# Kernel tuning notes

Hardware: AMD Instinct MI355X
Metric: run time of the kernel (lower is better)

Reference implementation:

```python
import jax, jax.numpy as jnp
import numpy as np

DIM = 1024          # hidden_size
MOE_HID = 512       # moe_intermediate_size
SHARED_HID = 2048   # shared_expert_intermediate_size
N_EXPERTS = 16
TOP_K = 2
NORM_TOPK_PROB = True


def setup_inputs() -> dict:
    key = jax.random.key(0)
    ks = jax.random.split(key, 9)
    s = 0.02  # init scale
    x = jax.random.normal(ks[0], (2, 1024, DIM), dtype=jnp.float32)
    Wg = jax.random.normal(ks[1], (N_EXPERTS, DIM), dtype=jnp.float32) * s
    We_gate = jax.random.normal(ks[2], (N_EXPERTS, MOE_HID, DIM), dtype=jnp.float32) * s
    We_up = jax.random.normal(ks[3], (N_EXPERTS, MOE_HID, DIM), dtype=jnp.float32) * s
    We_down = jax.random.normal(ks[4], (N_EXPERTS, DIM, MOE_HID), dtype=jnp.float32) * s
    Ws_gate = jax.random.normal(ks[5], (SHARED_HID, DIM), dtype=jnp.float32) * s
    Ws_up = jax.random.normal(ks[6], (SHARED_HID, DIM), dtype=jnp.float32) * s
    Ws_down = jax.random.normal(ks[7], (DIM, SHARED_HID), dtype=jnp.float32) * s
    Wsg = jax.random.normal(ks[8], (1, DIM), dtype=jnp.float32) * s
    return {"x": x, "Wg": Wg, "We_gate": We_gate, "We_up": We_up,
            "We_down": We_down, "Ws_gate": Ws_gate, "Ws_up": Ws_up,
            "Ws_down": Ws_down, "Wsg": Wsg}


def reference(x, Wg, We_gate, We_up, We_down, Ws_gate, Ws_up, Ws_down, Wsg):
    B, S, D = x.shape
    xt = x.reshape(-1, D)  # [T, D] tokens
    # router: softmax over experts, then top-k
    gates = jax.nn.softmax(xt @ Wg.T, axis=-1)          # [T, E]
    scores, inds = jax.lax.top_k(gates, TOP_K)           # [T, K]
    if NORM_TOPK_PROB:
        scores = scores / jnp.sum(scores, axis=-1, keepdims=True)
    # experts: SwiGLU computed for all experts, then gather the top-k outputs
    g = jnp.einsum('td,ehd->teh', xt, We_gate)           # [T, E, H]
    u = jnp.einsum('td,ehd->teh', xt, We_up)             # [T, E, H]
    h = jax.nn.silu(g) * u                               # swiglu
    y_all = jnp.einsum('teh,edh->ted', h, We_down)       # [T, E, D]
    y_sel = jnp.take_along_axis(y_all, inds[:, :, None], axis=1)  # [T, K, D]
    y = jnp.sum(y_sel * scores[:, :, None], axis=1)      # [T, D]
    # shared expert with sigmoid gate
    shared = (jax.nn.silu(xt @ Ws_gate.T) * (xt @ Ws_up.T)) @ Ws_down.T  # [T, D]
    y = y + jax.nn.sigmoid(xt @ Wsg.T) * shared
    return y.reshape(B, S, D)
```

## Files before the change

### kernel.cpp

```cpp
#include <hip/hip_runtime.h>
#include <stdint.h>

#define DIM 1024
#define MOE_HID 512
#define SH_HID 2048
#define NE 16
#define NT 2048
#define ROWS_CAP 6144

typedef unsigned short u16;
typedef __attribute__((ext_vector_type(8))) short s16x8;
typedef __attribute__((ext_vector_type(4))) float f32x4;

#define SYNC_BAR() \
  asm volatile("s_waitcnt lgkmcnt(0)" ::: "memory"); \
  __builtin_amdgcn_sched_barrier(0); \
  __builtin_amdgcn_s_barrier(); \
  __builtin_amdgcn_sched_barrier(0);

__device__ __forceinline__ u16 f2bf(float f){
  union { float f; unsigned v; } x; x.f = f;
  unsigned r = x.v + 0x7FFF + ((x.v >> 16) & 1);
  return (u16)(r >> 16);
}

__device__ __forceinline__ s16x8 cvt8pk(float4 a, float4 b){
  union { s16x8 v; unsigned u[4]; } r;
  asm volatile("v_cvt_pk_bf16_f32 %0, %1, %2" : "=v"(r.u[0]) : "v"(a.x), "v"(a.y));
  asm volatile("v_cvt_pk_bf16_f32 %0, %1, %2" : "=v"(r.u[1]) : "v"(a.z), "v"(a.w));
  asm volatile("v_cvt_pk_bf16_f32 %0, %1, %2" : "=v"(r.u[2]) : "v"(b.x), "v"(b.y));
  asm volatile("v_cvt_pk_bf16_f32 %0, %1, %2" : "=v"(r.u[3]) : "v"(b.z), "v"(b.w));
  return r.v;
}

__global__ void k_cvt_x(const float* __restrict__ s, u16* __restrict__ d){
  int i = (blockIdx.x * 256 + threadIdx.x) * 4;
  float4 v = *(const float4*)(s + i);
  ushort4 o;
  o.x = f2bf(v.x); o.y = f2bf(v.y); o.z = f2bf(v.z); o.w = f2bf(v.w);
  *(ushort4*)(d + i) = o;
}

__global__ void k_router(const float* __restrict__ x, const float* __restrict__ Wg,
                         const float* __restrict__ Wsgate1,
                         int* __restrict__ inds, float* __restrict__ scores,
                         float* __restrict__ gl){
  int lane = threadIdx.x & 63;
  int t = blockIdx.x * 4 + (threadIdx.x >> 6);
  const float4* xt = (const float4*)(x + (size_t)t * DIM);
  float4 xv[4];
#pragma unroll
  for(int j = 0; j < 4; j++) xv[j] = xt[lane + 64 * j];

  float acc[NE + 1];
#pragma unroll
  for(int e = 0; e <= NE; e++) acc[e] = 0.f;

#pragma unroll
  for(int e = 0; e < NE; e++){
    const float4* wr = (const float4*)(Wg + (size_t)e * DIM);
#pragma unroll
    for(int j = 0; j < 4; j++){
      float4 w = wr[lane + 64 * j];
      acc[e] += xv[j].x * w.x + xv[j].y * w.y + xv[j].z * w.z + xv[j].w * w.w;
    }
  }
  {
    const float4* wr = (const float4*)Wsgate1;
#pragma unroll
    for(int j = 0; j < 4; j++){
      float4 w = wr[lane + 64 * j];
      acc[NE] += xv[j].x * w.x + xv[j].y * w.y + xv[j].z * w.z + xv[j].w * w.w;
    }
  }

#pragma unroll
  for(int off = 32; off; off >>= 1)
#pragma unroll
    for(int e = 0; e <= NE; e++) acc[e] += __shfl_xor(acc[e], off, 64);

  if(lane == 0){
    int b0 = 0; float v0 = acc[0];
    for(int e = 1; e < NE; e++) if(acc[e] > v0){ v0 = acc[e]; b0 = e; }
    int b1 = (b0 == 0) ? 1 : 0; float v1 = acc[b1];
    for(int e = 0; e < NE; e++) if(e != b0 && acc[e] > v1){ v1 = acc[e]; b1 = e; }
    float s0 = 1.f / (1.f + __expf(v1 - v0));
    inds[t*2+0] = b0; inds[t*2+1] = b1;
    scores[t*2+0] = s0; scores[t*2+1] = 1.f - s0;
    gl[t] = acc[NE];
  }
}

__global__ void k_assign(const int* __restrict__ inds, const float* __restrict__ scores,
                         int* __restrict__ counts, int* __restrict__ offs,
                         int* __restrict__ tokrow, int* __restrict__ rowinfo,
                         float* __restrict__ rowscore){
  __shared__ int cnt[NE], off_s[NE], fill[NE];
  int tid = threadIdx.x;
  if(tid < NE){ cnt[tid] = 0; fill[tid] = 0; }
  __syncthreads();
  int ea[4];
#pragma unroll
  for(int i = 0; i < 4; i++){
    int a = tid + 1024 * i;
    ea[i] = inds[a];
    atomicAdd(&cnt[ea[i]], 1);
  }
  __syncthreads();
  if(tid == 0){
    int o = 0;
    for(int e = 0; e < NE; e++){
      off_s[e] = o;
      o += (cnt[e] + 127) & ~127;
    }
  }
  __syncthreads();
#pragma unroll
  for(int i = 0; i < 4; i++){
    int a = tid + 1024 * i;
    int e = ea[i];
    int row = off_s[e] + atomicAdd(&fill[e], 1);
    tokrow[a] = row;
    rowinfo[row] = a;
    rowscore[row] = scores[a];
  }
  if(tid < NE){ counts[tid] = cnt[tid]; offs[tid] = off_s[tid]; }
}

__global__ void k_scatter(const u16* __restrict__ xb, const int* __restrict__ tokrow,
                          u16* __restrict__ Xp){
  int t = blockIdx.x;
  int r0 = tokrow[t*2], r1 = tokrow[t*2+1];
  uint4 v = ((const uint4*)(xb + (size_t)t * DIM))[threadIdx.x];
  ((uint4*)(Xp + (size_t)r0 * DIM))[threadIdx.x] = v;
  ((uint4*)(Xp + (size_t)r1 * DIM))[threadIdx.x] = v;
}

__global__ __launch_bounds__(256, 2) void k_gateup_exp(
    const u16* __restrict__ Xp,
    const float* __restrict__ Weg, const float* __restrict__ Weu,
    u16* __restrict__ Hm,
    const int* __restrict__ counts, const int* __restrict__ offs){
  __shared__ __align__(16) u16 As[2][128 * 32];
  __shared__ __align__(16) u16 Bgs[2][64 * 32];
  __shared__ __align__(16) u16 Bus[2][64 * 32];

  const int row0 = blockIdx.y * 128;
  const int n0 = blockIdx.x * 64;
  const int rows_used = offs[NE-1] + ((counts[NE-1] + 127) & ~127);
  if(row0 >= rows_used) return;
  int e = 0;
#pragma unroll
  for(int k = 1; k < NE; k++) if(row0 >= offs[k]) e = k;

  const u16* A = Xp + (size_t)row0 * DIM;
  const float* Bg = Weg + (size_t)e * MOE_HID * DIM + (size_t)n0 * DIM;
  const float* Bu = Weu + (size_t)e * MOE_HID * DIM + (size_t)n0 * DIM;
  u16* H = Hm + (size_t)row0 * MOE_HID + n0;

  const int tid = threadIdx.x, lane = tid & 63, wid = tid >> 6;
  const int wm = wid >> 1, wn = wid & 1;
  const int srow = tid >> 2, p8 = (tid & 3) * 8;
  const int swz8 = (((tid & 3) ^ ((tid >> 3) & 3))) * 8;
  const int fr = lane & 15;
  const int fkswz = (((lane >> 4) ^ ((lane >> 1) & 3))) * 8;
  const int wA0 = srow * 32 + swz8, wA1 = (64 + srow) * 32 + swz8;
  const int wB = srow * 32 + swz8;

  const u16* Ar0 = A + (size_t)srow * DIM + p8;
  const u16* Ar1 = A + (size_t)(64 + srow) * DIM + p8;
  const float* Bgr = Bg + (size_t)srow * DIM + p8;
  const float* Bur = Bu + (size_t)srow * DIM + p8;

  uint4 aE0, aE1, aO0, aO1;
  float4 gE0, gE1, uE0, uE1, gO0, gO1, uO0, uO1;

#define GX_LOAD(S, ko) \
  a##S##0 = *(const uint4*)(Ar0 + (ko));  a##S##1 = *(const uint4*)(Ar1 + (ko)); \
  g##S##0 = *(const float4*)(Bgr + (ko)); g##S##1 = *(const float4*)(Bgr + (ko) + 4); \
  u##S##0 = *(const float4*)(Bur + (ko)); u##S##1 = *(const float4*)(Bur + (ko) + 4);

  f32x4 accg[4][2], accu[4][2];
#pragma unroll
  for(int m = 0; m < 4; m++)
#pragma unroll
    for(int n = 0; n < 2; n++){
      accg[m][n] = (f32x4){0.f,0.f,0.f,0.f};
      accu[m][n] = (f32x4){0.f,0.f,0.f,0.f};
    }

  GX_LOAD(E, 0)
  GX_LOAD(O, 32)

#define GX_STEP(tt, S, bb) { \
  *(uint4*)(As[bb] + wA0) = a##S##0; \
  *(uint4*)(As[bb] + wA1) = a##S##1; \
  *(s16x8*)(Bgs[bb] + wB) = cvt8pk(g##S##0, g##S##1); \
  *(s16x8*)(Bus[bb] + wB) = cvt8pk(u##S##0, u##S##1); \
  SYNC_BAR() \
  if((tt) + 2 < 32){ GX_LOAD(S, ((tt) + 2) * 32) } \
  s16x8 af[4], bgf[2], buf2[2]; \
  _Pragma("unroll") for(int m = 0; m < 4; m++) \
    af[m] = *(const s16x8*)(As[bb] + (wm*64 + m*16 + fr) * 32 + fkswz); \
  _Pragma("unroll") for(int n = 0; n < 2; n++){ \
    bgf[n]  = *(const s16x8*)(Bgs[bb] + (wn*32 + n*16 + fr) * 32 + fkswz); \
    buf2[n] = *(const s16x8*)(Bus[bb] + (wn*32 + n*16 + fr) * 32 + fkswz); } \
  _Pragma("unroll") for(int m = 0; m < 4; m++) \
  _Pragma("unroll") for(int n = 0; n < 2; n++){ \
    accg[m][n] = __builtin_amdgcn_mfma_f32_16x16x32_bf16(af[m], bgf[n], accg[m][n], 0, 0, 0); \
    accu[m][n] = __builtin_amdgcn_mfma_f32_16x16x32_bf16(af[m], buf2[n], accu[m][n], 0, 0, 0); } }

  for(int t = 0; t < 32; t += 2){
    GX_STEP(t,     E, 0)
    GX_STEP(t + 1, O, 1)
  }

#pragma unroll
  for(int m = 0; m < 4; m++)
#pragma unroll
    for(int n = 0; n < 2; n++)
#pragma unroll
      for(int i = 0; i < 4; i++){
        int r = wm*64 + m*16 + ((lane >> 4) << 2) + i;
        int c = wn*32 + n*16 + (lane & 15);
        float g = accg[m][n][i], u = accu[m][n][i];
        float h = (g / (1.f + __expf(-g))) * u;
        H[(size_t)r * MOE_HID + c] = f2bf(h);
      }
}

__global__ __launch_bounds__(256, 2) void k_gateup_sh(
    const u16* __restrict__ xb,
    const float* __restrict__ Wsg, const float* __restrict__ Wsu,
    u16* __restrict__ Hs){
  __shared__ __align__(16) u16 As[2][256 * 32];
  __shared__ __align__(16) u16 Bgs[2][64 * 32];
  __shared__ __align__(16) u16 Bus[2][64 * 32];

  const int mtile = blockIdx.y;
  const int n0 = blockIdx.x * 64;

  const u16* A = xb + (size_t)mtile * 256 * DIM;
  const float* Bg = Wsg + (size_t)n0 * DIM;
  const float* Bu = Wsu + (size_t)n0 * DIM;
  u16* H = Hs + (size_t)mtile * 256 * SH_HID + n0;

  const int tid = threadIdx.x, lane = tid & 63, wid = tid >> 6;
  const int wm = wid >> 1, wn = wid & 1;
  const int srow = tid >> 2, p8 = (tid & 3) * 8;
  const int swz8 = (((tid & 3) ^ ((tid >> 3) & 3))) * 8;
  const int fr = lane & 15;
  const int fkswz = (((lane >> 4) ^ ((lane >> 1) & 3))) * 8;
  const int wA0 = (srow      ) * 32 + swz8;
  const int wA1 = (srow +  64) * 32 + swz8;
  const int wA2 = (srow + 128) * 32 + swz8;
  const int wA3 = (srow + 192) * 32 + swz8;
  const int wB  = srow * 32 + swz8;

  const u16* Ar0 = A + (size_t)(srow      ) * DIM + p8;
  const u16* Ar1 = A + (size_t)(srow +  64) * DIM + p8;
  const u16* Ar2 = A + (size_t)(srow + 128) * DIM + p8;
  const u16* Ar3 = A + (size_t)(srow + 192) * DIM + p8;
  const float* Bgr = Bg + (size_t)srow * DIM + p8;
  const float* Bur = Bu + (size_t)srow * DIM + p8;

  uint4 aE0,aE1,aE2,aE3, aO0,aO1,aO2,aO3;
  float4 gE0,gE1,uE0,uE1, gO0,gO1,uO0,uO1;

#define GS_LOAD(S, ko) \
  a##S##0 = *(const uint4*)(Ar0 + (ko)); a##S##1 = *(const uint4*)(Ar1 + (ko)); \
  a##S##2 = *(const uint4*)(Ar2 + (ko)); a##S##3 = *(const uint4*)(Ar3 + (ko)); \
  g##S##0 = *(const float4*)(Bgr + (ko)); g##S##1 = *(const float4*)(Bgr + (ko) + 4); \
  u##S##0 = *(const float4*)(Bur + (ko)); u##S##1 = *(const float4*)(Bur + (ko) + 4);

  f32x4 accg[8][2], accu[8][2];
#pragma unroll
  for(int m = 0; m < 8; m++)
#pragma unroll
    for(int n = 0; n < 2; n++){
      accg[m][n] = (f32x4){0.f,0.f,0.f,0.f};
      accu[m][n] = (f32x4){0.f,0.f,0.f,0.f};
    }

  GS_LOAD(E, 0)
  GS_LOAD(O, 32)

#define GS_STEP(tt, S, bb) { \
  *(uint4*)(As[bb] + wA0) = a##S##0; \
  *(uint4*)(As[bb] + wA1) = a##S##1; \
  *(uint4*)(As[bb] + wA2) = a##S##2; \
  *(uint4*)(As[bb] + wA3) = a##S##3; \
  *(s16x8*)(Bgs[bb] + wB) = cvt8pk(g##S##0, g##S##1); \
  *(s16x8*)(Bus[bb] + wB) = cvt8pk(u##S##0, u##S##1); \
  SYNC_BAR() \
  if((tt) + 2 < 32){ GS_LOAD(S, ((tt) + 2) * 32) } \
  s16x8 af[8], bgf[2], buf2[2]; \
  _Pragma("unroll") for(int m = 0; m < 8; m++) \
    af[m] = *(const s16x8*)(As[bb] + (wm*128 + m*16 + fr) * 32 + fkswz); \
  _Pragma("unroll") for(int n = 0; n < 2; n++){ \
    bgf[n]  = *(const s16x8*)(Bgs[bb] + (wn*32 + n*16 + fr) * 32 + fkswz); \
    buf2[n] = *(const s16x8*)(Bus[bb] + (wn*32 + n*16 + fr) * 32 + fkswz); } \
  _Pragma("unroll") for(int m = 0; m < 8; m++) \
  _Pragma("unroll") for(int n = 0; n < 2; n++){ \
    accg[m][n] = __builtin_amdgcn_mfma_f32_16x16x32_bf16(af[m], bgf[n], accg[m][n], 0, 0, 0); \
    accu[m][n] = __builtin_amdgcn_mfma_f32_16x16x32_bf16(af[m], buf2[n], accu[m][n], 0, 0, 0); } }

  for(int t = 0; t < 32; t += 2){
    GS_STEP(t,     E, 0)
    GS_STEP(t + 1, O, 1)
  }

#pragma unroll
  for(int m = 0; m < 8; m++)
#pragma unroll
    for(int n = 0; n < 2; n++)
#pragma unroll
      for(int i = 0; i < 4; i++){
        int r = wm*128 + m*16 + ((lane >> 4) << 2) + i;
        int c = wn*32 + n*16 + (lane & 15);
        float g = accg[m][n][i], u = accu[m][n][i];
        float h = (g / (1.f + __expf(-g))) * u;
        H[(size_t)r * SH_HID + c] = f2bf(h);
      }
}

__global__ __launch_bounds__(256, 2) void k_down_all(
    const u16* __restrict__ Hm, const u16* __restrict__ Hs,
    const float* __restrict__ Wed, const float* __restrict__ Wsd,
    float* __restrict__ yp, float* __restrict__ Sh0, float* __restrict__ Sh1,
    const int* __restrict__ counts, const int* __restrict__ offs,
    const int* __restrict__ rowinfo, const float* __restrict__ rowscore){
  __shared__ __align__(16) u16 As[2][128 * 32];
  __shared__ __align__(16) u16 Bs[2][128 * 32];

  const int y = blockIdx.y, n0 = blockIdx.x * 128;
  const bool sh = (y < 32);
  const u16* A; const float* B; float* O = yp;
  int lda, M = NT, row0 = 0, kBeg = 0, nk, lrow = 0;
  if(sh){
    int mtile = y & 15, kz = y >> 4;
    A = Hs + (size_t)mtile * 128 * SH_HID; lda = SH_HID;
    B = Wsd; kBeg = kz * 1024; nk = 32;
    O = (kz == 0) ? Sh0 : Sh1;
    row0 = mtile * 128;
  } else {
    row0 = (y - 32) * 128;
    int rows_used = offs[NE-1] + ((counts[NE-1] + 127) & ~127);
    if(row0 >= rows_used) return;
    int e = 0;
#pragma unroll
    for(int k = 1; k < NE; k++) if(row0 >= offs[k]) e = k;
    M = counts[e];
    lrow = row0 - offs[e];
    A = Hm + (size_t)row0 * MOE_HID; lda = MOE_HID;
    B = Wed + (size_t)e * DIM * MOE_HID; nk = 16;
  }

  const int tid = threadIdx.x, lane = tid & 63, wid = tid >> 6;
  const int wm = wid >> 1, wn = wid & 1;
  const int srow = tid >> 2, p8 = (tid & 3) * 8;
  const int swz8 = (((tid & 3) ^ ((tid >> 3) & 3))) * 8;
  const int fr = lane & 15;
  const int fkswz = (((lane >> 4) ^ ((lane >> 1) & 3))) * 8;
  const int wA0 = srow * 32 + swz8, wA1 = (64 + srow) * 32 + swz8;

  const u16* Ar0 = A + (size_t)srow * lda + kBeg + p8;
  const u16* Ar1 = A + (size_t)(64 + srow) * lda + kBeg + p8;
  const float* Br0 = B + (size_t)(n0 + srow) * lda + kBeg + p8;
  const float* Br1 = B + (size_t)(n0 + 64 + srow) * lda + kBeg + p8;

  uint4 aE0, aE1, aO0, aO1;
  float4 bE00, bE01, bE10, bE11, bO00, bO01, bO10, bO11;

#define DN_LOAD(S, ko) \
  a##S##0 = *(const uint4*)(Ar0 + (ko));   a##S##1 = *(const uint4*)(Ar1 + (ko)); \
  b##S##00 = *(const float4*)(Br0 + (ko)); b##S##01 = *(const float4*)(Br0 + (ko) + 4); \
  b##S##10 = *(const float4*)(Br1 + (ko)); b##S##11 = *(const float4*)(Br1 + (ko) + 4);

  f32x4 acc[4][4];
#pragma unroll
  for(int m = 0; m < 4; m++)
#pragma unroll
    for(int n = 0; n < 4; n++) acc[m][n] = (f32x4){0.f,0.f,0.f,0.f};

  DN_LOAD(E, 0)
  DN_LOAD(O, 32)

#define DN_STEP(tt, S, bb) { \
  *(uint4*)(As[bb] + wA0) = a##S##0; \
  *(uint4*)(As[bb] + wA1) = a##S##1; \
  *(s16x8*)(Bs[bb] + wA0) = cvt8pk(b##S##00, b##S##01); \
  *(s16x8*)(Bs[bb] + wA1) = cvt8pk(b##S##10, b##S##11); \
  SYNC_BAR() \
  if((tt) + 2 < nk){ DN_LOAD(S, ((tt) + 2) * 32) } \
  s16x8 af[4], bf[4]; \
  _Pragma("unroll") for(int m = 0; m < 4; m++) \
    af[m] = *(const s16x8*)(As[bb] + (wm*64 + m*16 + fr) * 32 + fkswz); \
  _Pragma("unroll") for(int n = 0; n < 4; n++) \
    bf[n] = *(const s16x8*)(Bs[bb] + (wn*64 + n*16 + fr) * 32 + fkswz); \
  _Pragma("unroll") for(int m = 0; m < 4; m++) \
  _Pragma("unroll") for(int n = 0; n < 4; n++) \
    acc[m][n] = __builtin_amdgcn_mfma_f32_16x16x32_bf16(af[m], bf[n], acc[m][n], 0, 0, 0); }

  for(int t = 0; t < nk; t += 2){
    DN_STEP(t,     E, 0)
    DN_STEP(t + 1, O, 1)
  }

#pragma unroll
  for(int m = 0; m < 4; m++)
#pragma unroll
    for(int i = 0; i < 4; i++){
      int rl = wm*64 + m*16 + ((lane >> 4) << 2) + i;
      if(sh){
        float* orow = O + (size_t)(row0 + rl) * DIM + n0 + wn*64 + (lane & 15);
#pragma unroll
        for(int n = 0; n < 4; n++) orow[n*16] = acc[m][n][i];
      } else if(lrow + rl < M){
        int ar = row0 + rl;
        int slot = rowinfo[ar];
        float sc = rowscore[ar];
        float* orow = yp + (size_t)slot * DIM + n0 + wn*64 + (lane & 15);
#pragma unroll
        for(int n = 0; n < 4; n++) orow[n*16] = sc * acc[m][n][i];
      }
    }
}

__global__ void k_combine(const float* __restrict__ yp, const float* __restrict__ Sh0,
                          const float* __restrict__ Sh1,
                          const float* __restrict__ gl, float* __restrict__ out){
  int idx = (blockIdx.x * 256 + threadIdx.x) * 4;
  int t = idx >> 10;
  float s = 1.f / (1.f + __expf(-gl[t]));
  float4 a = *(const float4*)(yp + (size_t)(t*2)   * DIM + (idx & 1023));
  float4 b = *(const float4*)(yp + (size_t)(t*2+1) * DIM + (idx & 1023));
  float4 c0 = *(const float4*)(Sh0 + idx);
  float4 c1 = *(const float4*)(Sh1 + idx);
  float4 o;
  o.x = a.x + b.x + s * (c0.x + c1.x);
  o.y = a.y + b.y + s * (c0.y + c1.y);
  o.z = a.z + b.z + s * (c0.z + c1.z);
  o.w = a.w + b.w + s * (c0.w + c1.w);
  *(float4*)(out + idx) = o;
}

extern "C" void kernel_launch(void* const* d_in, const int* in_sizes, int n_in,
                              void* d_out, int out_size, void* d_ws, size_t ws_size,
                              hipStream_t stream){
  const float* x    = (const float*)d_in[0];
  const float* Wg   = (const float*)d_in[1];
  const float* Weg  = (const float*)d_in[2];
  const float* Weu  = (const float*)d_in[3];
  const float* Wed  = (const float*)d_in[4];
  const float* Wsg  = (const float*)d_in[5];
  const float* Wsu  = (const float*)d_in[6];
  const float* Wsd  = (const float*)d_in[7];
  const float* Wg1  = (const float*)d_in[8];
  float* out = (float*)d_out;

  char* p = (char*)d_ws;
  int* inds   = (int*)p;  p += 4096 * 4;
  float* scores = (float*)p; p += 4096 * 4;
  float* gl   = (float*)p;  p += NT * 4;
  int* counts = (int*)p;  p += 64;
  int* offs   = (int*)p;  p += 64;
  int* tokrow = (int*)p;  p += 4096 * 4;
  int* rowinfo = (int*)p; p += ROWS_CAP * 4;
  float* rowscore = (float*)p; p += ROWS_CAP * 4;
  u16* xb     = (u16*)p;  p += (size_t)NT * DIM * 2;
  u16* Hs     = (u16*)p;  p += (size_t)NT * SH_HID * 2;
  float* Sh0  = (float*)p; p += (size_t)NT * DIM * 4;
  float* Sh1  = (float*)p; p += (size_t)NT * DIM * 4;
  u16* Xp     = (u16*)p;  p += (size_t)ROWS_CAP * DIM * 2;
  u16* Hm     = (u16*)p;  p += (size_t)ROWS_CAP * MOE_HID * 2;
  float* yp   = (float*)p; p += (size_t)NT * 2 * DIM * 4;

  k_cvt_x<<<NT * DIM / (256 * 4), 256, 0, stream>>>(x, xb);
  k_router<<<NT/4, 256, 0, stream>>>(x, Wg, Wg1, inds, scores, gl);
  k_assign<<<1, 1024, 0, stream>>>(inds, scores, counts, offs, tokrow, rowinfo, rowscore);
  k_scatter<<<NT, 128, 0, stream>>>(xb, tokrow, Xp);

  k_gateup_exp<<<dim3(8, 48), 256, 0, stream>>>(Xp, Weg, Weu, Hm, counts, offs);
  k_gateup_sh<<<dim3(32, 8), 256, 0, stream>>>(xb, Wsg, Wsu, Hs);
  k_down_all<<<dim3(8, 80), 256, 0, stream>>>(Hm, Hs, Wed, Wsd,
                                              yp, Sh0, Sh1, counts, offs,
                                              rowinfo, rowscore);

  k_combine<<<2048, 256, 0, stream>>>(yp, Sh0, Sh1, gl, out);
}
```

Baseline: 128.4 us.

## Gather expert input rows directly in gate/up GEMM and widen K tile

Drops the scatter kernel that copied each token's bf16 row into a permuted expert buffer. The expert gate/up GEMM now reads rows straight from the token buffer via rowinfo indices, with padding rows clamped to token 0. The K tile is doubled from 32 to 64 with a new XOR swizzle, halving the number of barrier iterations at the cost of twice the LDS and more live registers. Router and convert launches are also reordered.

```diff
diff --git a/kernel.cpp b/kernel.cpp
--- a/kernel.cpp
+++ b/kernel.cpp
@@ -93,8 +93,7 @@
 
 __global__ void k_assign(const int* __restrict__ inds, const float* __restrict__ scores,
                          int* __restrict__ counts, int* __restrict__ offs,
-                         int* __restrict__ tokrow, int* __restrict__ rowinfo,
-                         float* __restrict__ rowscore){
+                         int* __restrict__ rowinfo, float* __restrict__ rowscore){
   __shared__ int cnt[NE], off_s[NE], fill[NE];
   int tid = threadIdx.x;
   if(tid < NE){ cnt[tid] = 0; fill[tid] = 0; }
@@ -120,30 +119,20 @@
     int a = tid + 1024 * i;
     int e = ea[i];
     int row = off_s[e] + atomicAdd(&fill[e], 1);
-    tokrow[a] = row;
     rowinfo[row] = a;
     rowscore[row] = scores[a];
   }
   if(tid < NE){ counts[tid] = cnt[tid]; offs[tid] = off_s[tid]; }
 }
 
-__global__ void k_scatter(const u16* __restrict__ xb, const int* __restrict__ tokrow,
-                          u16* __restrict__ Xp){
-  int t = blockIdx.x;
-  int r0 = tokrow[t*2], r1 = tokrow[t*2+1];
-  uint4 v = ((const uint4*)(xb + (size_t)t * DIM))[threadIdx.x];
-  ((uint4*)(Xp + (size_t)r0 * DIM))[threadIdx.x] = v;
-  ((uint4*)(Xp + (size_t)r1 * DIM))[threadIdx.x] = v;
-}
-
 __global__ __launch_bounds__(256, 2) void k_gateup_exp(
-    const u16* __restrict__ Xp,
+    const u16* __restrict__ xb, const int* __restrict__ rowinfo,
     const float* __restrict__ Weg, const float* __restrict__ Weu,
     u16* __restrict__ Hm,
     const int* __restrict__ counts, const int* __restrict__ offs){
-  __shared__ __align__(16) u16 As[2][128 * 32];
-  __shared__ __align__(16) u16 Bgs[2][64 * 32];
-  __shared__ __align__(16) u16 Bus[2][64 * 32];
+  __shared__ __align__(16) u16 As[2][128 * 64];
+  __shared__ __align__(16) u16 Bgs[2][64 * 64];
+  __shared__ __align__(16) u16 Bus[2][64 * 64];
 
   const int row0 = blockIdx.y * 128;
   const int n0 = blockIdx.x * 64;
@@ -153,32 +142,47 @@
 #pragma unroll
   for(int k = 1; k < NE; k++) if(row0 >= offs[k]) e = k;
 
-  const u16* A = Xp + (size_t)row0 * DIM;
   const float* Bg = Weg + (size_t)e * MOE_HID * DIM + (size_t)n0 * DIM;
   const float* Bu = Weu + (size_t)e * MOE_HID * DIM + (size_t)n0 * DIM;
   u16* H = Hm + (size_t)row0 * MOE_HID + n0;
 
   const int tid = threadIdx.x, lane = tid & 63, wid = tid >> 6;
   const int wm = wid >> 1, wn = wid & 1;
-  const int srow = tid >> 2, p8 = (tid & 3) * 8;
-  const int swz8 = (((tid & 3) ^ ((tid >> 3) & 3))) * 8;
+  const int srow = tid >> 2;
+  const int p16 = (tid & 3) * 16;
+  const int cb = (tid & 3) * 2;
+  const int key = srow & 7;
   const int fr = lane & 15;
-  const int fkswz = (((lane >> 4) ^ ((lane >> 1) & 3))) * 8;
-  const int wA0 = srow * 32 + swz8, wA1 = (64 + srow) * 32 + swz8;
-  const int wB = srow * 32 + swz8;
-
-  const u16* Ar0 = A + (size_t)srow * DIM + p8;
-  const u16* Ar1 = A + (size_t)(64 + srow) * DIM + p8;
-  const float* Bgr = Bg + (size_t)srow * DIM + p8;
-  const float* Bur = Bu + (size_t)srow * DIM + p8;
-
-  uint4 aE0, aE1, aO0, aO1;
-  float4 gE0, gE1, uE0, uE1, gO0, gO1, uO0, uO1;
+  const int fc = lane >> 4;
+  const int fx = fr & 7;
+
+  const int wA00 = (srow     ) * 64 + ((cb    ) ^ key) * 8;
+  const int wA01 = (srow     ) * 64 + ((cb + 1) ^ key) * 8;
+  const int wA10 = (srow + 64) * 64 + ((cb    ) ^ key) * 8;
+  const int wA11 = (srow + 64) * 64 + ((cb + 1) ^ key) * 8;
+  const int wB0  = srow * 64 + ((cb    ) ^ key) * 8;
+  const int wB1  = srow * 64 + ((cb + 1) ^ key) * 8;
+
+  int a0 = rowinfo[row0 + srow];
+  int a1 = rowinfo[row0 + 64 + srow];
+  int t0 = ((unsigned)a0 < 4096u) ? (a0 >> 1) : 0;
+  int t1 = ((unsigned)a1 < 4096u) ? (a1 >> 1) : 0;
+  const u16* Ar0 = xb + (size_t)t0 * DIM + p16;
+  const u16* Ar1 = xb + (size_t)t1 * DIM + p16;
+  const float* Bgr = Bg + (size_t)srow * DIM + p16;
+  const float* Bur = Bu + (size_t)srow * DIM + p16;
+
+  uint4 aE00, aE01, aE10, aE11, aO00, aO01, aO10, aO11;
+  float4 gE0, gE1, gE2, gE3, uE0, uE1, uE2, uE3;
+  float4 gO0, gO1, gO2, gO3, uO0, uO1, uO2, uO3;
 
 #define GX_LOAD(S, ko) \
-  a##S##0 = *(const uint4*)(Ar0 + (ko));  a##S##1 = *(const uint4*)(Ar1 + (ko)); \
-  g##S##0 = *(const float4*)(Bgr + (ko)); g##S##1 = *(const float4*)(Bgr + (ko) + 4); \
-  u##S##0 = *(const float4*)(Bur + (ko)); u##S##1 = *(const float4*)(Bur + (ko) + 4);
+  a##S##00 = *(const uint4*)(Ar0 + (ko));      a##S##01 = *(const uint4*)(Ar0 + (ko) + 8); \
+  a##S##10 = *(const uint4*)(Ar1 + (ko));      a##S##11 = *(const uint4*)(Ar1 + (ko) + 8); \
+  g##S##0 = *(const float4*)(Bgr + (ko));      g##S##1 = *(const float4*)(Bgr + (ko) + 4); \
+  g##S##2 = *(const float4*)(Bgr + (ko) + 8);  g##S##3 = *(const float4*)(Bgr + (ko) + 12); \
+  u##S##0 = *(const float4*)(Bur + (ko));      u##S##1 = *(const float4*)(Bur + (ko) + 4); \
+  u##S##2 = *(const float4*)(Bur + (ko) + 8);  u##S##3 = *(const float4*)(Bur + (ko) + 12);
 
   f32x4 accg[4][2], accu[4][2];
 #pragma unroll
@@ -190,27 +194,37 @@
     }
 
   GX_LOAD(E, 0)
-  GX_LOAD(O, 32)
+  GX_LOAD(O, 64)
 
 #define GX_STEP(tt, S, bb) { \
-  *(uint4*)(As[bb] + wA0) = a##S##0; \
-  *(uint4*)(As[bb] + wA1) = a##S##1; \
-  *(s16x8*)(Bgs[bb] + wB) = cvt8pk(g##S##0, g##S##1); \
-  *(s16x8*)(Bus[bb] + wB) = cvt8pk(u##S##0, u##S##1); \
+  *(uint4*)(As[bb] + wA00) = a##S##00; \
+  *(uint4*)(As[bb] + wA01) = a##S##01; \
+  *(uint4*)(As[bb] + wA10) = a##S##10; \
+  *(uint4*)(As[bb] + wA11) = a##S##11; \
+  *(s16x8*)(Bgs[bb] + wB0) = cvt8pk(g##S##0, g##S##1); \
+  *(s16x8*)(Bgs[bb] + wB1) = cvt8pk(g##S##2, g##S##3); \
+  *(s16x8*)(Bus[bb] + wB0) = cvt8pk(u##S##0, u##S##1); \
+  *(s16x8*)(Bus[bb] + wB1) = cvt8pk(u##S##2, u##S##3); \
   SYNC_BAR() \
-  if((tt) + 2 < 32){ GX_LOAD(S, ((tt) + 2) * 32) } \
-  s16x8 af[4], bgf[2], buf2[2]; \
-  _Pragma("unroll") for(int m = 0; m < 4; m++) \
-    af[m] = *(const s16x8*)(As[bb] + (wm*64 + m*16 + fr) * 32 + fkswz); \
+  if((tt) + 2 < 16){ GX_LOAD(S, ((tt) + 2) * 64) } \
+  s16x8 af[4][2], bgf[2][2], buf2[2][2]; \
+  _Pragma("unroll") for(int m = 0; m < 4; m++){ \
+    int r = wm*64 + m*16 + fr; \
+    _Pragma("unroll") for(int ks = 0; ks < 2; ks++) \
+      af[m][ks] = *(const s16x8*)(As[bb] + r*64 + (((ks*4 + fc) ^ fx)) * 8); } \
   _Pragma("unroll") for(int n = 0; n < 2; n++){ \
-    bgf[n]  = *(const s16x8*)(Bgs[bb] + (wn*32 + n*16 + fr) * 32 + fkswz); \
-    buf2[n] = *(const s16x8*)(Bus[bb] + (wn*32 + n*16 + fr) * 32 + fkswz); } \
+    int r = wn*32 + n*16 + fr; \
+    _Pragma("unroll") for(int ks = 0; ks < 2; ks++){ \
+      bgf[n][ks]  = *(const s16x8*)(Bgs[bb] + r*64 + (((ks*4 + fc) ^ fx)) * 8); \
+      buf2[n][ks] = *(const s16x8*)(Bus[bb] + r*64 + (((ks*4 + fc) ^ fx)) * 8); } } \
   _Pragma("unroll") for(int m = 0; m < 4; m++) \
   _Pragma("unroll") for(int n = 0; n < 2; n++){ \
-    accg[m][n] = __builtin_amdgcn_mfma_f32_16x16x32_bf16(af[m], bgf[n], accg[m][n], 0, 0, 0); \
-    accu[m][n] = __builtin_amdgcn_mfma_f32_16x16x32_bf16(af[m], buf2[n], accu[m][n], 0, 0, 0); } }
-
-  for(int t = 0; t < 32; t += 2){
+    accg[m][n] = __builtin_amdgcn_mfma_f32_16x16x32_bf16(af[m][0], bgf[n][0], accg[m][n], 0, 0, 0); \
+    accg[m][n] = __builtin_amdgcn_mfma_f32_16x16x32_bf16(af[m][1], bgf[n][1], accg[m][n], 0, 0, 0); \
+    accu[m][n] = __builtin_amdgcn_mfma_f32_16x16x32_bf16(af[m][0], buf2[n][0], accu[m][n], 0, 0, 0); \
+    accu[m][n] = __builtin_amdgcn_mfma_f32_16x16x32_bf16(af[m][1], buf2[n][1], accu[m][n], 0, 0, 0); } }
+
+  for(int t = 0; t < 16; t += 2){
     GX_STEP(t,     E, 0)
     GX_STEP(t + 1, O, 1)
   }
@@ -465,23 +479,20 @@
   float* gl   = (float*)p;  p += NT * 4;
   int* counts = (int*)p;  p += 64;
   int* offs   = (int*)p;  p += 64;
-  int* tokrow = (int*)p;  p += 4096 * 4;
   int* rowinfo = (int*)p; p += ROWS_CAP * 4;
   float* rowscore = (float*)p; p += ROWS_CAP * 4;
   u16* xb     = (u16*)p;  p += (size_t)NT * DIM * 2;
   u16* Hs     = (u16*)p;  p += (size_t)NT * SH_HID * 2;
   float* Sh0  = (float*)p; p += (size_t)NT * DIM * 4;
   float* Sh1  = (float*)p; p += (size_t)NT * DIM * 4;
-  u16* Xp     = (u16*)p;  p += (size_t)ROWS_CAP * DIM * 2;
   u16* Hm     = (u16*)p;  p += (size_t)ROWS_CAP * MOE_HID * 2;
   float* yp   = (float*)p; p += (size_t)NT * 2 * DIM * 4;
 
+  k_router<<<NT/4, 256, 0, stream>>>(x, Wg, Wg1, inds, scores, gl);
   k_cvt_x<<<NT * DIM / (256 * 4), 256, 0, stream>>>(x, xb);
-  k_router<<<NT/4, 256, 0, stream>>>(x, Wg, Wg1, inds, scores, gl);
-  k_assign<<<1, 1024, 0, stream>>>(inds, scores, counts, offs, tokrow, rowinfo, rowscore);
-  k_scatter<<<NT, 128, 0, stream>>>(xb, tokrow, Xp);
-
-  k_gateup_exp<<<dim3(8, 48), 256, 0, stream>>>(Xp, Weg, Weu, Hm, counts, offs);
+  k_assign<<<1, 1024, 0, stream>>>(inds, scores, counts, offs, rowinfo, rowscore);
+
+  k_gateup_exp<<<dim3(8, 48), 256, 0, stream>>>(xb, rowinfo, Weg, Weu, Hm, counts, offs);
   k_gateup_sh<<<dim3(32, 8), 256, 0, stream>>>(xb, Wsg, Wsu, Hs);
   k_down_all<<<dim3(8, 80), 256, 0, stream>>>(Hm, Hs, Wed, Wsd,
                                               yp, Sh0, Sh1, counts, offs,
```

Result: faster. 123.1 us (-4.2%).
